# Optimization experiments

Hardware: AMD Instinct MI355X
Metric: run time of the kernel (lower is better)

Reference implementation:

```python
import jax, jax.numpy as jnp
import numpy as np

B, L, D = 2, 4096, 1024
H, DK, DV = 4, 256, 256
CONV_K, FIR_S, FIR_L = 4, 3, 31
CHUNK = 32
EPS = 1e-5


def l2norm(x):
    return x * jax.lax.rsqrt(jnp.sum(x * x, -1, keepdims=True) + 1e-6)


def causal_dwconv(x, w):
    # x: [B, L, C], w: [C, K] depthwise causal FIR conv (left pad K-1)
    C, K = w.shape
    y = jax.lax.conv_general_dilated(
        jnp.swapaxes(x, 1, 2), w[:, None, :], (1,), [(K - 1, 0)],
        feature_group_count=C, dimension_numbers=('NCH', 'OIH', 'NCH'))
    return jnp.swapaxes(y, 1, 2)


def delta_rule_chunkwise(q, k, v, beta, chunk=CHUNK):
    # q,k: [b,h,L,dk], v: [b,h,L,dv], beta: [b,h,L]
    b, h, Lx, dk = q.shape
    dv = v.shape[-1]
    pad = (-Lx) % chunk
    if pad:
        q, k, v = (jnp.pad(t, ((0, 0), (0, 0), (0, pad), (0, 0))) for t in (q, k, v))
        beta = jnp.pad(beta, ((0, 0), (0, 0), (0, pad)))
    Lp = Lx + pad
    n = Lp // chunk
    q = l2norm(q)
    k = l2norm(k)
    v = v * beta[..., None]
    k_beta = k * beta[..., None]
    ch = lambda t: t.reshape(b, h, n, chunk, -1)
    qc, kc, vc, kbc = map(ch, (q, k, v, k_beta))
    # UT transform: T = (I + strictly_lower(k_beta @ k^T))^{-1}
    A = jnp.einsum('bhncd,bhned->bhnce', kbc, kc)
    eye = jnp.eye(chunk, dtype=q.dtype)
    T = jnp.linalg.inv(eye + jnp.tril(A, -1))  # same math as the sequential forward-substitution loop
    u = T @ vc      # [b,h,n,c,dv]
    w = T @ kbc     # [b,h,n,c,dk]
    tri = jnp.tril(jnp.ones((chunk, chunk), bool))  # causal incl. diagonal

    def body(S, inp):
        q_i, k_i, u_i, w_i = inp
        attn = jnp.where(tri, jnp.einsum('bhcd,bhed->bhce', q_i, k_i), 0.)
        u_i = u_i - w_i @ S
        o_i = q_i @ S + attn @ u_i
        S = S + jnp.einsum('bhcd,bhce->bhde', k_i, u_i)
        return S, o_i

    mv = lambda t: jnp.moveaxis(t, 2, 0)
    S0 = jnp.zeros((b, h, dk, dv), q.dtype)
    S, o = jax.lax.scan(body, S0, (mv(qc), mv(kc), mv(u), mv(w)))
    o = jnp.moveaxis(o, 0, 2).reshape(b, h, Lp, dv)[:, :, :Lx]
    return o, S


def setup_inputs() -> dict:
    key = jax.random.key(0)
    ks = jax.random.split(key, 16)
    s = 0.02
    fir_short = jnp.zeros((H, DV, FIR_S)).at[..., -1].set(1.0) + 1e-3 * jax.random.normal(ks[8], (H, DV, FIR_S))
    fir_long = jnp.zeros((H, DV, FIR_L)).at[..., -1].set(1.0) + 1e-3 * jax.random.normal(ks[9], (H, DV, FIR_L))
    bl = jnp.zeros((H, 3)).at[:, 0].set(2.0).reshape(-1)  # value_path_bias
    return dict(
        hidden_states=jax.random.normal(ks[0], (B, L, D), jnp.float32),
        Wq=s * jax.random.normal(ks[1], (D, H * DK)),
        Wk=s * jax.random.normal(ks[2], (D, H * DK)),
        Wv=s * jax.random.normal(ks[3], (D, H * DV)),
        conv_q=0.3 * jax.random.normal(ks[4], (H * DK, CONV_K)),
        conv_k=0.3 * jax.random.normal(ks[5], (H * DK, CONV_K)),
        conv_v=0.3 * jax.random.normal(ks[6], (H * DV, CONV_K)),
        Wb=s * jax.random.normal(ks[7], (D, H)),
        fir_short=fir_short,
        fir_long=fir_long,
        Wg=s * jax.random.normal(ks[10], (D, H)),
        bg=0.5 * jnp.ones((H,)),  # global_gate_bias
        Wl=s * jax.random.normal(ks[11], (D, H * 3)),
        bl=bl,
        log_temp=jnp.ones((H,)),  # log(e * temp_init) with temp_init=1
        rms_w=jnp.ones((DV,)),
        Wo=s * jax.random.normal(ks[12], (H * DV, D)),
    )


def reference(hidden_states, Wq, Wk, Wv, conv_q, conv_k, conv_v, Wb,
              fir_short, fir_long, Wg, bg, Wl, bl, log_temp, rms_w, Wo):
    x = hidden_states
    Bx, Lx, _ = x.shape
    # q/k/v projections + causal short conv + SiLU (qk_activation='silu')
    q = jax.nn.silu(causal_dwconv(x @ Wq, conv_q)).reshape(Bx, Lx, H, DK)
    k = jax.nn.silu(causal_dwconv(x @ Wk, conv_k)).reshape(Bx, Lx, H, DK)
    v = jax.nn.silu(causal_dwconv(x @ Wv, conv_v)).reshape(Bx, Lx, H, DV)
    beta = jax.nn.sigmoid(x @ Wb)  # [B,L,H]
    o_d, S = delta_rule_chunkwise(
        q.transpose(0, 2, 1, 3), k.transpose(0, 2, 1, 3),
        v.transpose(0, 2, 1, 3), beta.transpose(0, 2, 1))
    delta_out = o_d.transpose(0, 2, 1, 3)  # [B,L,H,DV]
    # local FIR paths on v (per-head depthwise causal FIR)
    vf = v.reshape(Bx, Lx, H * DV)
    local_short = causal_dwconv(vf, fir_short.reshape(H * DV, FIR_S)).reshape(Bx, Lx, H, DV)
    local_long = causal_dwconv(vf, fir_long.reshape(H * DV, FIR_L)).reshape(Bx, Lx, H, DV)
    # hierarchical two-stage gating with learnable per-head temperature
    w_global = jax.nn.sigmoid(x @ Wg + bg)  # [B,L,H]
    temp = jnp.exp(log_temp)                # [H]
    logits = (x @ Wl + bl).reshape(Bx, Lx, H, 3) / temp[:, None]
    p = jax.nn.softmax(logits, axis=-1)
    local_mix = p[..., 0:1] * v + p[..., 1:2] * local_short + p[..., 2:3] * local_long
    o = w_global[..., None] * delta_out + (1.0 - w_global)[..., None] * local_mix
    # per-head RMSNorm then output projection
    o = o * jax.lax.rsqrt(jnp.mean(o * o, -1, keepdims=True) + EPS) * rms_w
    return o.reshape(Bx, Lx, H * DV) @ Wo
```

## Files before the change

### kernel.cpp

```cpp
#include <hip/hip_runtime.h>
#include <hip/hip_bf16.h>
#include <math.h>

#define Bn 2
#define Ln 4096
#define Dn 1024
#define Hn 4
#define DKn 256
#define DVn 256
#define NCHn 128

typedef __attribute__((ext_vector_type(8))) short short8;
typedef __attribute__((ext_vector_type(4))) float f32x4;

__device__ __forceinline__ float sigmoidf_(float x) { return 1.f / (1.f + __expf(-x)); }

__device__ __forceinline__ unsigned short f2bf(float f) {
  union { float f; unsigned u; } v; v.f = f;
  unsigned r = v.u + 0x7FFFu + ((v.u >> 16) & 1u);
  return (unsigned short)(r >> 16);
}

__device__ __forceinline__ float bf2f(unsigned short u) {
  union { unsigned u; float f; } v; v.u = ((unsigned)u) << 16;
  return v.f;
}

__device__ __forceinline__ unsigned cvt_pk_bf16(float a, float b) {
  unsigned r;
  asm volatile("v_cvt_pk_bf16_f32 %0, %1, %2" : "=v"(r) : "v"(a), "v"(b));
  return r;
}

__device__ __forceinline__ short8 pack_i4(int4 o) {
  short8 r;
  __builtin_memcpy(&r, &o, 16);
  return r;
}

__device__ __forceinline__ void gl2lds16(const void* g, void* l) {
  __builtin_amdgcn_global_load_lds((const __attribute__((address_space(1))) unsigned int*)g,
                                   (__attribute__((address_space(3))) unsigned int*)l, 16, 0, 0);
}

__global__ __launch_bounds__(256) void wt_all_kernel(
    const float* __restrict__ W0, const float* __restrict__ W1,
    const float* __restrict__ W2, const float* __restrict__ W3,
    unsigned short* __restrict__ T0, unsigned short* __restrict__ T1,
    unsigned short* __restrict__ T2, unsigned short* __restrict__ T3) {
  const float* W = (blockIdx.z == 0) ? W0 : (blockIdx.z == 1) ? W1
                   : (blockIdx.z == 2) ? W2 : W3;
  unsigned short* Wt = (blockIdx.z == 0) ? T0 : (blockIdx.z == 1) ? T1
                       : (blockIdx.z == 2) ? T2 : T3;
  __shared__ float tile[32][33];
  const int bx = blockIdx.x * 32;
  const int by = blockIdx.y * 32;
  const int tx = threadIdx.x & 31, ty4 = (threadIdx.x >> 5) * 4;
#pragma unroll
  for (int r = 0; r < 4; ++r)
    tile[ty4 + r][tx] = W[(size_t)(by + ty4 + r) * 1024 + bx + tx];
  __syncthreads();
#pragma unroll
  for (int r = 0; r < 4; ++r)
    Wt[(size_t)(bx + ty4 + r) * 1024 + by + tx] = f2bf(tile[tx][ty4 + r]);
}

template <int OBF>
__global__ __launch_bounds__(256, 2) void gemm_bf16(const unsigned short* __restrict__ A,
                                                    const unsigned short* __restrict__ Bt,
                                                    void* __restrict__ Cv,
                                                    int M, int N, int K) {
  __shared__ __align__(16) unsigned short As[128 * 32];
  __shared__ __align__(16) unsigned short Bs[128 * 32];
  const int tid = threadIdx.x;
  const int wid = tid >> 6, lane = tid & 63;
  const int row0 = blockIdx.y * 128, col0 = blockIdx.x * 128;
  const int wr64 = (wid >> 1) * 64, wc64 = (wid & 1) * 64;
  const int fr = lane & 15, fg = lane >> 4;
  f32x4 acc[4][4];
#pragma unroll
  for (int i = 0; i < 4; ++i)
#pragma unroll
    for (int j = 0; j < 4; ++j) acc[i][j] = (f32x4){0.f, 0.f, 0.f, 0.f};
  for (int k0 = 0; k0 < K; k0 += 32) {
#pragma unroll
    for (int i = 0; i < 2; ++i) {
      const int off = wid * 2048 + i * 1024 + (lane << 4);
      const int r = off >> 6;
      const int kb = off & 63;
      gl2lds16((const char*)A + ((size_t)(row0 + r) * K + k0) * 2 + kb, (char*)As + off);
      gl2lds16((const char*)Bt + ((size_t)(col0 + r) * K + k0) * 2 + kb, (char*)Bs + off);
    }
    __syncthreads();
    short8 a[4], b[4];
#pragma unroll
    for (int mi = 0; mi < 4; ++mi)
      a[mi] = *(const short8*)&As[(wr64 + mi * 16 + fr) * 32 + fg * 8];
#pragma unroll
    for (int ni = 0; ni < 4; ++ni)
      b[ni] = *(const short8*)&Bs[(wc64 + ni * 16 + fr) * 32 + fg * 8];
#pragma unroll
    for (int mi = 0; mi < 4; ++mi)
#pragma unroll
      for (int ni = 0; ni < 4; ++ni)
        acc[mi][ni] = __builtin_amdgcn_mfma_f32_16x16x32_bf16(a[mi], b[ni], acc[mi][ni], 0, 0, 0);
    __syncthreads();
  }
#pragma unroll
  for (int mi = 0; mi < 4; ++mi) {
    const int orow = row0 + wr64 + mi * 16 + fg * 4;
#pragma unroll
    for (int ni = 0; ni < 4; ++ni) {
      const int ocol = col0 + wc64 + ni * 16 + fr;
      if (OBF) {
        unsigned short* C = (unsigned short*)Cv;
#pragma unroll
        for (int r = 0; r < 4; ++r)
          C[(size_t)(orow + r) * N + ocol] = f2bf(acc[mi][ni][r]);
      } else {
        float* C = (float*)Cv;
#pragma unroll
        for (int r = 0; r < 4; ++r)
          C[(size_t)(orow + r) * N + ocol] = acc[mi][ni][r];
      }
    }
  }
}

__global__ __launch_bounds__(256) void gates_kernel(
    const float* __restrict__ x, const float* __restrict__ Wb,
    const float* __restrict__ Wg, const float* __restrict__ bg,
    const float* __restrict__ Wl, const float* __restrict__ bl,
    const float* __restrict__ log_temp, float* __restrict__ beta,
    float* __restrict__ wgl, float* __restrict__ pmix,
    unsigned short* __restrict__ xb) {
  const int wave = threadIdx.x >> 6, lane = threadIdx.x & 63;
  const int row = (blockIdx.x << 2) + wave;
  if (row >= Bn * Ln) return;
  const float* xr = x + (size_t)row * Dn;
  float acc[20];
#pragma unroll
  for (int c = 0; c < 20; ++c) acc[c] = 0.f;
#pragma unroll
  for (int i = 0; i < 4; ++i) {
    const float4 xv = *(const float4*)&xr[(lane << 2) + (i << 8)];
    ushort4 ob;
    ob.x = f2bf(xv.x); ob.y = f2bf(xv.y); ob.z = f2bf(xv.z); ob.w = f2bf(xv.w);
    *(ushort4*)&xb[(size_t)row * Dn + (i << 8) + (lane << 2)] = ob;
    const float xa[4] = {xv.x, xv.y, xv.z, xv.w};
#pragma unroll
    for (int j = 0; j < 4; ++j) {
      const int kk = (i << 8) + (lane << 2) + j;
      const float xx = xa[j];
#pragma unroll
      for (int h = 0; h < 4; ++h) acc[h] = fmaf(xx, Wb[kk * 4 + h], acc[h]);
#pragma unroll
      for (int h = 0; h < 4; ++h) acc[4 + h] = fmaf(xx, Wg[kk * 4 + h], acc[4 + h]);
#pragma unroll
      for (int c = 0; c < 12; ++c) acc[8 + c] = fmaf(xx, Wl[kk * 12 + c], acc[8 + c]);
    }
  }
#pragma unroll
  for (int c = 0; c < 20; ++c)
    for (int off = 32; off; off >>= 1) acc[c] += __shfl_down(acc[c], off);
  if (lane == 0) {
    const int b = row >> 12, l = row & (Ln - 1);
#pragma unroll
    for (int h = 0; h < 4; ++h)
      beta[((size_t)(b * Hn + h) << 12) + l] = sigmoidf_(acc[h]);
#pragma unroll
    for (int h = 0; h < 4; ++h) wgl[row * 4 + h] = sigmoidf_(acc[4 + h] + bg[h]);
#pragma unroll
    for (int h = 0; h < 4; ++h) {
      const float it = 1.f / __expf(log_temp[h]);
      const float l0 = (acc[8 + h * 3 + 0] + bl[h * 3 + 0]) * it;
      const float l1 = (acc[8 + h * 3 + 1] + bl[h * 3 + 1]) * it;
      const float l2 = (acc[8 + h * 3 + 2] + bl[h * 3 + 2]) * it;
      const float mx = fmaxf(l0, fmaxf(l1, l2));
      const float e0 = __expf(l0 - mx), e1 = __expf(l1 - mx), e2 = __expf(l2 - mx);
      const float is = 1.f / (e0 + e1 + e2);
      pmix[row * 12 + h * 3 + 0] = e0 * is;
      pmix[row * 12 + h * 3 + 1] = e1 * is;
      pmix[row * 12 + h * 3 + 2] = e2 * is;
    }
  }
}

#define CLT 16
__global__ __launch_bounds__(384) void conv_fused_kernel(
    const unsigned short* __restrict__ qkv, const float* __restrict__ cq,
    const float* __restrict__ ck, const float* __restrict__ cv,
    unsigned short* __restrict__ qn, unsigned short* __restrict__ kn,
    unsigned short* __restrict__ vn) {
  const int wgid = ((int)blockIdx.x & 7) * 64 + ((int)blockIdx.x >> 3);
  const int b = wgid >> 8;
  const int lt = wgid & 255;
  const int l0 = lt * CLT;
  const int t = threadIdx.x;
  const int tensor = t >> 7;
  const int head = (t & 127) >> 5;
  const int ch0 = (t & 31) * 8;
  const int col = tensor * 1024 + head * 256 + ch0;
  const float* cw = (tensor == 0) ? cq : (tensor == 1) ? ck : cv;
  float w4[8][4];
#pragma unroll
  for (int e = 0; e < 8; ++e)
#pragma unroll
    for (int j = 0; j < 4; ++j) w4[e][j] = cw[(head * 256 + ch0 + e) * 4 + j];
  float h0[8], h1[8], h2[8];
#pragma unroll
  for (int e = 0; e < 8; ++e) { h0[e] = 0.f; h1[e] = 0.f; h2[e] = 0.f; }
  {
    const int ls0 = l0 - 3;
    if (ls0 >= 0) {
      const short8 r = *(const short8*)&qkv[(((size_t)b << 12) + ls0) * 3072 + col];
#pragma unroll
      for (int e = 0; e < 8; ++e) h0[e] = bf2f((unsigned short)r[e]);
    }
    if (l0 - 2 >= 0) {
      const short8 r = *(const short8*)&qkv[(((size_t)b << 12) + l0 - 2) * 3072 + col];
#pragma unroll
      for (int e = 0; e < 8; ++e) h1[e] = bf2f((unsigned short)r[e]);
    }
    if (l0 - 1 >= 0) {
      const short8 r = *(const short8*)&qkv[(((size_t)b << 12) + l0 - 1) * 3072 + col];
#pragma unroll
      for (int e = 0; e < 8; ++e) h2[e] = bf2f((unsigned short)r[e]);
    }
  }
  unsigned short* outp = (tensor == 0) ? qn : (tensor == 1) ? kn : vn;
  const size_t obase = (((size_t)(b * Hn + head)) << 12) * 256 + ch0;
#pragma unroll
  for (int i = 0; i < CLT; ++i) {
    const int l = l0 + i;
    const short8 r = *(const short8*)&qkv[(((size_t)b << 12) + l) * 3072 + col];
    float cur[8], a[8];
#pragma unroll
    for (int e = 0; e < 8; ++e) cur[e] = bf2f((unsigned short)r[e]);
    float ssq = 0.f;
#pragma unroll
    for (int e = 0; e < 8; ++e) {
      float s = w4[e][3] * cur[e];
      s = fmaf(w4[e][0], h0[e], s);
      s = fmaf(w4[e][1], h1[e], s);
      s = fmaf(w4[e][2], h2[e], s);
      const float y = s * sigmoidf_(s);
      a[e] = y;
      ssq = fmaf(y, y, ssq);
      h0[e] = h1[e]; h1[e] = h2[e]; h2[e] = cur[e];
    }
    float sc = 1.f;
    if (tensor < 2) {
#pragma unroll
      for (int m = 1; m <= 16; m <<= 1) ssq += __shfl_xor(ssq, m);
      sc = rsqrtf(ssq + 1e-6f);
    }
    short8 o;
#pragma unroll
    for (int e = 0; e < 8; ++e) o[e] = (short)f2bf(a[e] * sc);
    *(short8*)&outp[obase + (size_t)l * 256] = o;
  }
}

__global__ __launch_bounds__(256, 2) void precomp_kernel(
    const unsigned short* __restrict__ q, const unsigned short* __restrict__ k,
    const unsigned short* __restrict__ v, const float* __restrict__ beta,
    unsigned short* __restrict__ wfrag, unsigned short* __restrict__ qfrag,
    unsigned short* __restrict__ ktfrag, unsigned short* __restrict__ afrag,
    float* __restrict__ u0frag) {
  const int blk = blockIdx.x;
  const int n = blk & 127, bh = blk >> 7;
  const size_t base = (((size_t)bh << 12) + (n << 5)) * 256;
  const size_t cid = (size_t)(bh * NCHn + n);
  __shared__ __align__(16) unsigned short ksb[32][264];
  __shared__ __align__(16) unsigned short qsb[32][264];
  __shared__ __align__(16) unsigned short vbb[32][264];
  __shared__ float Tm[32][33], Am[32][33], bet[32];
  __shared__ __align__(16) float attn_l[32][36];
  const int t = threadIdx.x;
  const int wid = t >> 6, lane = t & 63;
  const int fr = lane & 15, fg = lane >> 4;
  if (t < 32) bet[t] = beta[((size_t)bh << 12) + (n << 5) + t];
#pragma unroll
  for (int it = 0; it < 4; ++it) {
    const int idx = t + it * 256;
    const int r = idx >> 5, c8 = (idx & 31) << 3;
    const float bv = beta[((size_t)bh << 12) + (n << 5) + r];
    *(int4*)&qsb[r][c8] = *(const int4*)&q[base + r * 256 + c8];
    *(int4*)&ksb[r][c8] = *(const int4*)&k[base + r * 256 + c8];
    const int4 vv = *(const int4*)&v[base + r * 256 + c8];
    const unsigned vu[4] = {(unsigned)vv.x, (unsigned)vv.y, (unsigned)vv.z, (unsigned)vv.w};
    int4 ov;
    ov.x = cvt_pk_bf16(bf2f((unsigned short)(vu[0] & 0xffff)) * bv,
                       bf2f((unsigned short)(vu[0] >> 16)) * bv);
    ov.y = cvt_pk_bf16(bf2f((unsigned short)(vu[1] & 0xffff)) * bv,
                       bf2f((unsigned short)(vu[1] >> 16)) * bv);
    ov.z = cvt_pk_bf16(bf2f((unsigned short)(vu[2] & 0xffff)) * bv,
                       bf2f((unsigned short)(vu[2] >> 16)) * bv);
    ov.w = cvt_pk_bf16(bf2f((unsigned short)(vu[3] & 0xffff)) * bv,
                       bf2f((unsigned short)(vu[3] >> 16)) * bv);
    *(int4*)&vbb[r][c8] = ov;
  }
  __syncthreads();
  {
    const int ti = wid >> 1, tj = wid & 1;
    f32x4 G = (f32x4){0.f, 0.f, 0.f, 0.f};
    f32x4 At = (f32x4){0.f, 0.f, 0.f, 0.f};
#pragma unroll
    for (int kw = 0; kw < 8; ++kw) {
      const short8 krow = *(const short8*)&ksb[ti * 16 + fr][kw * 32 + fg * 8];
      const short8 kcol = *(const short8*)&ksb[tj * 16 + fr][kw * 32 + fg * 8];
      const short8 qrow = *(const short8*)&qsb[ti * 16 + fr][kw * 32 + fg * 8];
      G = __builtin_amdgcn_mfma_f32_16x16x32_bf16(krow, kcol, G, 0, 0, 0);
      At = __builtin_amdgcn_mfma_f32_16x16x32_bf16(qrow, kcol, At, 0, 0, 0);
    }
#pragma unroll
    for (int r_ = 0; r_ < 4; ++r_) {
      const int i = ti * 16 + fg * 4 + r_;
      const int j = tj * 16 + fr;
      Am[i][j] = bet[i] * G[r_];
      attn_l[i][j] = (j <= i) ? At[r_] : 0.f;
    }
  }
#pragma unroll
  for (int it = 0; it < 4; ++it) {
    const int u = it * 4 + wid;
    const int mi = u >> 3, kw = u & 7;
    *(int4*)&qfrag[cid * 8192 + u * 512 + lane * 8] =
        *(const int4*)&qsb[mi * 16 + fr][kw * 32 + fg * 8];
  }
#pragma unroll
  for (int it = 0; it < 4; ++it) {
    const int mi = it * 4 + wid;
    const int dk = mi * 16 + fr;
    unsigned short e[8];
#pragma unroll
    for (int j = 0; j < 8; ++j) e[j] = ksb[fg * 8 + j][dk];
    int4 o;
    o.x = e[0] | ((unsigned)e[1] << 16);
    o.y = e[2] | ((unsigned)e[3] << 16);
    o.z = e[4] | ((unsigned)e[5] << 16);
    o.w = e[6] | ((unsigned)e[7] << 16);
    *(int4*)&ktfrag[cid * 8192 + mi * 512 + lane * 8] = o;
  }
  __syncthreads();
  if (t >= 128) {
    const int mi = (t >> 6) - 2;
    const int c = mi * 16 + fr;
    const float4 a = *(const float4*)&attn_l[c][fg * 8];
    const float4 b2 = *(const float4*)&attn_l[c][fg * 8 + 4];
    int4 o;
    o.x = f2bf(a.x) | ((unsigned)f2bf(a.y) << 16);
    o.y = f2bf(a.z) | ((unsigned)f2bf(a.w) << 16);
    o.z = f2bf(b2.x) | ((unsigned)f2bf(b2.y) << 16);
    o.w = f2bf(b2.z) | ((unsigned)f2bf(b2.w) << 16);
    *(int4*)&afrag[cid * 1024 + mi * 512 + lane * 8] = o;
  }
  if (t < 32) {
    float Tcol[32];
    Tcol[0] = (t == 0) ? 1.f : 0.f;
#pragma unroll
    for (int i = 1; i < 32; ++i) {
      float s0 = 0.f, s1 = 0.f;
      int m = 0;
#pragma unroll
      for (; m + 2 <= i; m += 2) {
        s0 = fmaf(Am[i][m], Tcol[m], s0);
        s1 = fmaf(Am[i][m + 1], Tcol[m + 1], s1);
      }
      if (m < i) s0 = fmaf(Am[i][m], Tcol[m], s0);
      Tcol[i] = ((i == t) ? 1.f : 0.f) - s0 - s1;
    }
#pragma unroll
    for (int i = 0; i < 32; ++i) Tm[i][t] = Tcol[i];
  }
  __syncthreads();
  {
    float betr[8];
#pragma unroll
    for (int j = 0; j < 8; ++j) betr[j] = bet[fg * 8 + j];
    short8 Tf[2], Tbf[2];
#pragma unroll
    for (int mi = 0; mi < 2; ++mi) {
      float tv[8];
#pragma unroll
      for (int j = 0; j < 8; ++j) tv[j] = Tm[mi * 16 + fr][fg * 8 + j];
      int4 p, pb;
      p.x = cvt_pk_bf16(tv[0], tv[1]); p.y = cvt_pk_bf16(tv[2], tv[3]);
      p.z = cvt_pk_bf16(tv[4], tv[5]); p.w = cvt_pk_bf16(tv[6], tv[7]);
      pb.x = cvt_pk_bf16(tv[0] * betr[0], tv[1] * betr[1]);
      pb.y = cvt_pk_bf16(tv[2] * betr[2], tv[3] * betr[3]);
      pb.z = cvt_pk_bf16(tv[4] * betr[4], tv[5] * betr[5]);
      pb.w = cvt_pk_bf16(tv[6] * betr[6], tv[7] * betr[7]);
      Tf[mi] = pack_i4(p);
      Tbf[mi] = pack_i4(pb);
    }
    const f32x4 zero = (f32x4){0.f, 0.f, 0.f, 0.f};
#pragma unroll
    for (int tt = 0; tt < 4; ++tt) {
      const int tjc = wid * 4 + tt;
      unsigned short ev[8], ek[8];
#pragma unroll
      for (int j = 0; j < 8; ++j) {
        ev[j] = vbb[fg * 8 + j][tjc * 16 + fr];
        ek[j] = ksb[fg * 8 + j][tjc * 16 + fr];
      }
      int4 pv, pk;
      pv.x = ev[0] | ((unsigned)ev[1] << 16); pv.y = ev[2] | ((unsigned)ev[3] << 16);
      pv.z = ev[4] | ((unsigned)ev[5] << 16); pv.w = ev[6] | ((unsigned)ev[7] << 16);
      pk.x = ek[0] | ((unsigned)ek[1] << 16); pk.y = ek[2] | ((unsigned)ek[3] << 16);
      pk.z = ek[4] | ((unsigned)ek[5] << 16); pk.w = ek[6] | ((unsigned)ek[7] << 16);
      const short8 vbf = pack_i4(pv);
      const short8 kbf = pack_i4(pk);
#pragma unroll
      for (int mi = 0; mi < 2; ++mi) {
        const f32x4 U = __builtin_amdgcn_mfma_f32_16x16x32_bf16(Tf[mi], vbf, zero, 0, 0, 0);
        *(f32x4*)&u0frag[cid * 8192 + (tjc * 2 + mi) * 256 + lane * 4] = U;
        const f32x4 W = __builtin_amdgcn_mfma_f32_16x16x32_bf16(Tbf[mi], kbf, zero, 0, 0, 0);
#pragma unroll
        for (int r_ = 0; r_ < 4; ++r_)
          qsb[mi * 16 + fg * 4 + r_][tjc * 16 + fr] = f2bf(W[r_]);
      }
    }
  }
  __syncthreads();
#pragma unroll
  for (int it = 0; it < 4; ++it) {
    const int u = it * 4 + wid;
    const int mi = u >> 3, kw = u & 7;
    *(int4*)&wfrag[cid * 8192 + u * 512 + lane * 8] =
        *(const int4*)&qsb[mi * 16 + fr][kw * 32 + fg * 8];
  }
}

__global__ __launch_bounds__(128, 1) void scan_mfma(
    const unsigned short* __restrict__ wfrag, const unsigned short* __restrict__ qfrag,
    const unsigned short* __restrict__ ktfrag, const unsigned short* __restrict__ afrag,
    const float* __restrict__ u0frag, unsigned short* __restrict__ dout) {
  const int bh = blockIdx.x & 7;
  const int dvs = blockIdx.x >> 3;
  const int tid = threadIdx.x;
  const int w = tid >> 6;
  const int lane = tid & 63;
  const int fr = lane & 15, fg = lane >> 4;
  const int swz = (fr & 7) << 4;
  __shared__ __align__(16) unsigned short St[2][2048];
  __shared__ __align__(16) unsigned short ut2[2][512];
  __shared__ __align__(16) float pux[2][2][2][256];
  __shared__ __align__(16) float pox[2][2][2][256];
  f32x4 S[8];
#pragma unroll
  for (int i = 0; i < 8; ++i) S[i] = (f32x4){0.f, 0.f, 0.f, 0.f};

  const unsigned short* wbase = wfrag + (size_t)(bh * NCHn) * 8192;
  const unsigned short* qbase = qfrag + (size_t)(bh * NCHn) * 8192;
  const unsigned short* kbase = ktfrag + (size_t)(bh * NCHn) * 8192;
  const unsigned short* abase = afrag + (size_t)(bh * NCHn) * 1024;
  const float* ubase = u0frag + (size_t)(bh * NCHn) * 8192 + dvs * 512;

  short8 wr[8], qr[8], ktr[8];
  short8 ar[2] = {};
  f32x4 u0r[2];
#pragma unroll
  for (int u8 = 0; u8 < 8; ++u8) {
    const int mi = u8 >> 2, kwp = u8 & 3;
    const int u = mi * 8 + 4 * w + kwp;
    wr[u8] = *(const short8*)&wbase[u * 512 + lane * 8];
    qr[u8] = *(const short8*)&qbase[u * 512 + lane * 8];
    ktr[u8] = *(const short8*)&kbase[(8 * w + u8) * 512 + lane * 8];
  }
#pragma unroll
  for (int u = 0; u < 2; ++u) u0r[u] = *(const f32x4*)&ubase[u * 256 + lane * 4];
  if (w == 0) {
#pragma unroll
    for (int u = 0; u < 2; ++u) ar[u] = *(const short8*)&abase[u * 512 + lane * 8];
  }

  for (int n = 0; n < NCHn; ++n) {
    const int np = (n + 1 < NCHn) ? (n + 1) : n;
    const int buf = n & 1;
#pragma unroll
    for (int mi = 0; mi < 8; ++mi) {
      const unsigned w0 = cvt_pk_bf16(S[mi][0], S[mi][1]);
      const unsigned w1 = cvt_pk_bf16(S[mi][2], S[mi][3]);
      const int a = (fr * 256 + mi * 32 + fg * 8) ^ swz;
      *(uint2*)((char*)&St[w][0] + a) = make_uint2(w0, w1);
    }
    short8 sb[4];
#pragma unroll
    for (int kwp = 0; kwp < 4; ++kwp) {
      const int a = (fr * 256 + kwp * 64 + fg * 16) ^ swz;
      sb[kwp] = *(const short8*)((const char*)&St[w][0] + a);
    }
    f32x4 up[2], oq[2];
    up[0] = up[1] = (f32x4){0.f, 0.f, 0.f, 0.f};
    oq[0] = oq[1] = (f32x4){0.f, 0.f, 0.f, 0.f};
#pragma unroll
    for (int kwp = 0; kwp < 4; ++kwp) {
#pragma unroll
      for (int mi = 0; mi < 2; ++mi) {
        up[mi] = __builtin_amdgcn_mfma_f32_16x16x32_bf16(wr[mi * 4 + kwp], sb[kwp], up[mi], 0, 0, 0);
        oq[mi] = __builtin_amdgcn_mfma_f32_16x16x32_bf16(qr[mi * 4 + kwp], sb[kwp], oq[mi], 0, 0, 0);
      }
    }
    {
      const unsigned short* wp = wbase + (size_t)np * 8192;
      const unsigned short* qp = qbase + (size_t)np * 8192;
#pragma unroll
      for (int u8 = 0; u8 < 8; ++u8) {
        const int mi = u8 >> 2, kwp = u8 & 3;
        const int u = mi * 8 + 4 * w + kwp;
        wr[u8] = *(const short8*)&wp[u * 512 + lane * 8];
        qr[u8] = *(const short8*)&qp[u * 512 + lane * 8];
      }
    }
#pragma unroll
    for (int mi = 0; mi < 2; ++mi) {
      *(f32x4*)&pux[w][buf][mi][lane * 4] = up[mi];
      *(f32x4*)&pox[w][buf][mi][lane * 4] = oq[mi];
    }
    asm volatile("s_waitcnt lgkmcnt(0)" ::: "memory");
    __builtin_amdgcn_s_barrier();
    __builtin_amdgcn_sched_barrier(0);
    f32x4 o_f[2];
#pragma unroll
    for (int mi = 0; mi < 2; ++mi) {
      const f32x4 puo = *(const f32x4*)&pux[w ^ 1][buf][mi][lane * 4];
      const f32x4 uu = u0r[mi] - up[mi] - puo;
      const unsigned a0 = cvt_pk_bf16(uu[0], uu[1]);
      const unsigned a1 = cvt_pk_bf16(uu[2], uu[3]);
      const int ad = (fr * 64 + mi * 32 + fg * 8) ^ swz;
      *(uint2*)((char*)&ut2[w][0] + ad) = make_uint2(a0, a1);
      o_f[mi] = oq[mi] + *(const f32x4*)&pox[w ^ 1][buf][mi][lane * 4];
    }
    asm volatile("s_waitcnt lgkmcnt(0)" ::: "memory");
    __builtin_amdgcn_sched_barrier(0);
    const short8 ub = *(const short8*)((const char*)&ut2[w][0] + ((fr * 64 + fg * 16) ^ swz));
    if (w == 0) {
#pragma unroll
      for (int mi = 0; mi < 2; ++mi)
        o_f[mi] = __builtin_amdgcn_mfma_f32_16x16x32_bf16(ar[mi], ub, o_f[mi], 0, 0, 0);
      const unsigned short* ap = abase + (size_t)np * 1024;
#pragma unroll
      for (int u = 0; u < 2; ++u) ar[u] = *(const short8*)&ap[u * 512 + lane * 8];
      const size_t cb = ((size_t)((bh << 12) + (n << 5))) * 256;
#pragma unroll
      for (int mi = 0; mi < 2; ++mi)
#pragma unroll
        for (int r = 0; r < 4; ++r)
          dout[cb + (size_t)(mi * 16 + fg * 4 + r) * 256 + dvs * 16 + fr] = f2bf(o_f[mi][r]);
    }
    {
      const float* up_ = ubase + (size_t)np * 8192;
#pragma unroll
      for (int u = 0; u < 2; ++u) u0r[u] = *(const f32x4*)&up_[u * 256 + lane * 4];
    }
#pragma unroll
    for (int mi = 0; mi < 8; ++mi)
      S[mi] = __builtin_amdgcn_mfma_f32_16x16x32_bf16(ktr[mi], ub, S[mi], 0, 0, 0);
    {
      const unsigned short* kp = kbase + (size_t)np * 8192;
#pragma unroll
      for (int u8 = 0; u8 < 8; ++u8)
        ktr[u8] = *(const short8*)&kp[(8 * w + u8) * 512 + lane * 8];
    }
  }
}

#define MIX_LT 16
__global__ __launch_bounds__(256) void mix_kernel(
    const unsigned short* __restrict__ v, const unsigned short* __restrict__ delta,
    const float* __restrict__ wgl, const float* __restrict__ pmix,
    const float* __restrict__ firs, const float* __restrict__ firl,
    const float* __restrict__ rms_w, unsigned short* __restrict__ out) {
  const int wgid = ((int)blockIdx.x & 7) * 256 + ((int)blockIdx.x >> 3);
  const int b = wgid >> 10;
  const int h = (wgid >> 8) & 3;
  const int lt = wgid & 255;
  const int l0 = lt * MIX_LT;
  const int t = threadIdx.x;
  const int wv = t >> 6, lane = t & 63;
  const unsigned short* vcol = v + ((((size_t)(b * Hn + h)) << 12)) * 256 + t;
  const unsigned short* dcol = delta + ((((size_t)(b * Hn + h)) << 12)) * 256 + t;
  float fw[31], fs3[3];
#pragma unroll
  for (int j = 0; j < 31; ++j) fw[j] = firl[((h << 8) + t) * 31 + j];
#pragma unroll
  for (int j = 0; j < 3; ++j) fs3[j] = firs[((h << 8) + t) * 3 + j];
  const float rw = rms_w[t];
  float vbuf[46];
#pragma unroll
  for (int j = 0; j < 30; ++j) {
    const int ls = l0 - 30 + j;
    vbuf[j] = (ls >= 0) ? bf2f(vcol[(size_t)ls * 256]) : 0.f;
  }
#pragma unroll
  for (int i = 0; i < MIX_LT; ++i) vbuf[30 + i] = bf2f(vcol[(size_t)(l0 + i) * 256]);
  __shared__ float wred[MIX_LT * 4];
  float o[MIX_LT];
#pragma unroll
  for (int i = 0; i < MIX_LT; ++i) {
    const int l = l0 + i;
    const float vnew = vbuf[30 + i];
    float lo = fw[30] * vnew;
#pragma unroll
    for (int j = 0; j < 30; ++j) lo = fmaf(fw[j], vbuf[i + j], lo);
    float sh = fs3[2] * vnew;
    sh = fmaf(fs3[1], vbuf[i + 29], sh);
    sh = fmaf(fs3[0], vbuf[i + 28], sh);
    const int row = (b << 12) + l;
    const float p0 = pmix[row * 12 + h * 3 + 0];
    const float p1 = pmix[row * 12 + h * 3 + 1];
    const float p2 = pmix[row * 12 + h * 3 + 2];
    const float wg = wgl[row * 4 + h];
    const float mixv = p0 * vnew + p1 * sh + p2 * lo;
    const float oo = wg * bf2f(dcol[(size_t)l * 256]) + (1.f - wg) * mixv;
    o[i] = oo;
    float ss = oo * oo;
#pragma unroll
    for (int m = 1; m < 64; m <<= 1) ss += __shfl_xor(ss, m);
    if (lane == 0) wred[i * 4 + wv] = ss;
  }
  __syncthreads();
#pragma unroll
  for (int i = 0; i < MIX_LT; ++i) {
    const float sum = wred[i * 4] + wred[i * 4 + 1] + wred[i * 4 + 2] + wred[i * 4 + 3];
    const float sc = rsqrtf(sum * (1.f / 256.f) + 1e-5f);
    const int l = l0 + i;
    out[(size_t)((b << 12) + l) * 1024 + (h << 8) + t] = f2bf(o[i] * sc * rw);
  }
}

extern "C" void kernel_launch(void* const* d_in, const int* in_sizes, int n_in,
                              void* d_out, int out_size, void* d_ws, size_t ws_size,
                              hipStream_t stream) {
  const float* x = (const float*)d_in[0];
  const float* Wq = (const float*)d_in[1];
  const float* Wk = (const float*)d_in[2];
  const float* Wv = (const float*)d_in[3];
  const float* cq = (const float*)d_in[4];
  const float* ck = (const float*)d_in[5];
  const float* cv = (const float*)d_in[6];
  const float* Wb = (const float*)d_in[7];
  const float* firs = (const float*)d_in[8];
  const float* firl = (const float*)d_in[9];
  const float* Wg = (const float*)d_in[10];
  const float* bg = (const float*)d_in[11];
  const float* Wl = (const float*)d_in[12];
  const float* bl = (const float*)d_in[13];
  const float* ltemp = (const float*)d_in[14];
  const float* rmsw = (const float*)d_in[15];
  const float* Wo = (const float*)d_in[16];

  float* ws = (float*)d_ws;
  const size_t NE = (size_t)Bn * Ln * 1024;
  unsigned short* qkvbf = (unsigned short*)ws;
  unsigned short* wfrag = (unsigned short*)ws;
  unsigned short* qfrag = wfrag + 8388608;
  unsigned short* ktfrag = (unsigned short*)(ws + NE);
  unsigned short* afrag = ktfrag + 8388608;
  float* u0frag = ws + 2 * NE;
  unsigned short* xb = (unsigned short*)(ws + 3 * NE);
  unsigned short* normed_bf = xb;
  unsigned short* Wqt = xb + NE;
  unsigned short* Wkt = Wqt + 1048576;
  unsigned short* Wvt = Wkt + 1048576;
  unsigned short* qn_bf = (unsigned short*)(ws + 4 * NE);
  unsigned short* kn_bf = qn_bf + NE;
  unsigned short* vn_bf = (unsigned short*)(ws + 5 * NE);
  unsigned short* dout_bf = vn_bf + NE;
  float* beta = ws + 6 * NE;
  float* wgl = beta + (size_t)Bn * Hn * Ln;
  float* pmix = wgl + (size_t)Bn * Ln * Hn;
  unsigned short* Wot = (unsigned short*)(pmix + (size_t)Bn * Ln * Hn * 3);

  wt_all_kernel<<<dim3(32, 32, 4), 256, 0, stream>>>(Wq, Wk, Wv, Wo,
                                                     Wqt, Wkt, Wvt, Wot);
  gates_kernel<<<Bn * Ln / 4, 256, 0, stream>>>(x, Wb, Wg, bg, Wl, bl, ltemp,
                                                beta, wgl, pmix, xb);
  gemm_bf16<1><<<dim3(24, 64), 256, 0, stream>>>(xb, Wqt, qkvbf, Bn * Ln, 3072, 1024);
  conv_fused_kernel<<<Bn * (Ln / CLT), 384, 0, stream>>>(qkvbf, cq, ck, cv,
                                                         qn_bf, kn_bf, vn_bf);
  precomp_kernel<<<Bn * Hn * NCHn, 256, 0, stream>>>(qn_bf, kn_bf, vn_bf, beta,
                                                     wfrag, qfrag, ktfrag, afrag,
                                                     u0frag);
  scan_mfma<<<128, 128, 0, stream>>>(wfrag, qfrag, ktfrag, afrag, u0frag, dout_bf);
  mix_kernel<<<Bn * Hn * (Ln / MIX_LT), 256, 0, stream>>>(
      vn_bf, dout_bf, wgl, pmix, firs, firl, rmsw, normed_bf);
  gemm_bf16<0><<<dim3(8, 64), 256, 0, stream>>>(normed_bf, Wot, (float*)d_out,
                                                Bn * Ln, 1024, 1024);
}
```

Before: 372.3 us.

## Split scan state across four waves instead of two per workgroup

The sequential chunk scan now runs with 256 threads (4 waves) per block instead of 128, so each wave owns 64 rows of the dk dimension of the state S instead of 128. Each wave therefore does half the MFMAs and fragment loads per chunk on the serial critical path. In exchange, the cross-wave partial-sum reduction through shared memory grows from one to three partner reads. Only wave 0 now gathers the output partials, and more waves must take part in each per-chunk barrier.

```diff
diff --git a/kernel.cpp b/kernel.cpp
--- a/kernel.cpp
+++ b/kernel.cpp
@@ -211,9 +211,8 @@
 #pragma unroll
   for (int e = 0; e < 8; ++e) { h0[e] = 0.f; h1[e] = 0.f; h2[e] = 0.f; }
   {
-    const int ls0 = l0 - 3;
-    if (ls0 >= 0) {
-      const short8 r = *(const short8*)&qkv[(((size_t)b << 12) + ls0) * 3072 + col];
+    if (l0 - 3 >= 0) {
+      const short8 r = *(const short8*)&qkv[(((size_t)b << 12) + l0 - 3) * 3072 + col];
 #pragma unroll
       for (int e = 0; e < 8; ++e) h0[e] = bf2f((unsigned short)r[e]);
     }
@@ -433,7 +432,7 @@
   }
 }
 
-__global__ __launch_bounds__(128, 1) void scan_mfma(
+__global__ __launch_bounds__(256, 1) void scan_mfma(
     const unsigned short* __restrict__ wfrag, const unsigned short* __restrict__ qfrag,
     const unsigned short* __restrict__ ktfrag, const unsigned short* __restrict__ afrag,
     const float* __restrict__ u0frag, unsigned short* __restrict__ dout) {
@@ -444,13 +443,13 @@
   const int lane = tid & 63;
   const int fr = lane & 15, fg = lane >> 4;
   const int swz = (fr & 7) << 4;
-  __shared__ __align__(16) unsigned short St[2][2048];
-  __shared__ __align__(16) unsigned short ut2[2][512];
-  __shared__ __align__(16) float pux[2][2][2][256];
-  __shared__ __align__(16) float pox[2][2][2][256];
-  f32x4 S[8];
-#pragma unroll
-  for (int i = 0; i < 8; ++i) S[i] = (f32x4){0.f, 0.f, 0.f, 0.f};
+  __shared__ __align__(16) unsigned short St[4][1024];
+  __shared__ __align__(16) unsigned short ut2[4][512];
+  __shared__ __align__(16) float pux[4][2][2][256];
+  __shared__ __align__(16) float pox[4][2][2][256];
+  f32x4 S[4];
+#pragma unroll
+  for (int i = 0; i < 4; ++i) S[i] = (f32x4){0.f, 0.f, 0.f, 0.f};
 
   const unsigned short* wbase = wfrag + (size_t)(bh * NCHn) * 8192;
   const unsigned short* qbase = qfrag + (size_t)(bh * NCHn) * 8192;
@@ -458,17 +457,20 @@
   const unsigned short* abase = afrag + (size_t)(bh * NCHn) * 1024;
   const float* ubase = u0frag + (size_t)(bh * NCHn) * 8192 + dvs * 512;
 
-  short8 wr[8], qr[8], ktr[8];
+  short8 wr[2][2], qr[2][2], ktr[4];
   short8 ar[2] = {};
   f32x4 u0r[2];
 #pragma unroll
-  for (int u8 = 0; u8 < 8; ++u8) {
-    const int mi = u8 >> 2, kwp = u8 & 3;
-    const int u = mi * 8 + 4 * w + kwp;
-    wr[u8] = *(const short8*)&wbase[u * 512 + lane * 8];
-    qr[u8] = *(const short8*)&qbase[u * 512 + lane * 8];
-    ktr[u8] = *(const short8*)&kbase[(8 * w + u8) * 512 + lane * 8];
-  }
+  for (int mi2 = 0; mi2 < 2; ++mi2)
+#pragma unroll
+    for (int kwp = 0; kwp < 2; ++kwp) {
+      const int u = mi2 * 8 + 2 * w + kwp;
+      wr[mi2][kwp] = *(const short8*)&wbase[u * 512 + lane * 8];
+      qr[mi2][kwp] = *(const short8*)&qbase[u * 512 + lane * 8];
+    }
+#pragma unroll
+  for (int j = 0; j < 4; ++j)
+    ktr[j] = *(const short8*)&kbase[(4 * w + j) * 512 + lane * 8];
 #pragma unroll
   for (int u = 0; u < 2; ++u) u0r[u] = *(const f32x4*)&ubase[u * 256 + lane * 4];
   if (w == 0) {
@@ -480,75 +482,84 @@
     const int np = (n + 1 < NCHn) ? (n + 1) : n;
     const int buf = n & 1;
 #pragma unroll
-    for (int mi = 0; mi < 8; ++mi) {
-      const unsigned w0 = cvt_pk_bf16(S[mi][0], S[mi][1]);
-      const unsigned w1 = cvt_pk_bf16(S[mi][2], S[mi][3]);
-      const int a = (fr * 256 + mi * 32 + fg * 8) ^ swz;
+    for (int j = 0; j < 4; ++j) {
+      const unsigned w0 = cvt_pk_bf16(S[j][0], S[j][1]);
+      const unsigned w1 = cvt_pk_bf16(S[j][2], S[j][3]);
+      const int a = (fr * 128 + j * 32 + fg * 8) ^ swz;
       *(uint2*)((char*)&St[w][0] + a) = make_uint2(w0, w1);
     }
-    short8 sb[4];
-#pragma unroll
-    for (int kwp = 0; kwp < 4; ++kwp) {
-      const int a = (fr * 256 + kwp * 64 + fg * 16) ^ swz;
+    short8 sb[2];
+#pragma unroll
+    for (int kwp = 0; kwp < 2; ++kwp) {
+      const int a = (fr * 128 + kwp * 64 + fg * 16) ^ swz;
       sb[kwp] = *(const short8*)((const char*)&St[w][0] + a);
     }
     f32x4 up[2], oq[2];
     up[0] = up[1] = (f32x4){0.f, 0.f, 0.f, 0.f};
     oq[0] = oq[1] = (f32x4){0.f, 0.f, 0.f, 0.f};
 #pragma unroll
-    for (int kwp = 0; kwp < 4; ++kwp) {
-#pragma unroll
-      for (int mi = 0; mi < 2; ++mi) {
-        up[mi] = __builtin_amdgcn_mfma_f32_16x16x32_bf16(wr[mi * 4 + kwp], sb[kwp], up[mi], 0, 0, 0);
-        oq[mi] = __builtin_amdgcn_mfma_f32_16x16x32_bf16(qr[mi * 4 + kwp], sb[kwp], oq[mi], 0, 0, 0);
+    for (int kwp = 0; kwp < 2; ++kwp) {
+#pragma unroll
+      for (int mi2 = 0; mi2 < 2; ++mi2) {
+        up[mi2] = __builtin_amdgcn_mfma_f32_16x16x32_bf16(wr[mi2][kwp], sb[kwp], up[mi2], 0, 0, 0);
+        oq[mi2] = __builtin_amdgcn_mfma_f32_16x16x32_bf16(qr[mi2][kwp], sb[kwp], oq[mi2], 0, 0, 0);
       }
     }
     {
       const unsigned short* wp = wbase + (size_t)np * 8192;
       const unsigned short* qp = qbase + (size_t)np * 8192;
 #pragma unroll
-      for (int u8 = 0; u8 < 8; ++u8) {
-        const int mi = u8 >> 2, kwp = u8 & 3;
-        const int u = mi * 8 + 4 * w + kwp;
-        wr[u8] = *(const short8*)&wp[u * 512 + lane * 8];
-        qr[u8] = *(const short8*)&qp[u * 512 + lane * 8];
-      }
-    }
-#pragma unroll
-    for (int mi = 0; mi < 2; ++mi) {
-      *(f32x4*)&pux[w][buf][mi][lane * 4] = up[mi];
-      *(f32x4*)&pox[w][buf][mi][lane * 4] = oq[mi];
+      for (int mi2 = 0; mi2 < 2; ++mi2)
+#pragma unroll
+        for (int kwp = 0; kwp < 2; ++kwp) {
+          const int u = mi2 * 8 + 2 * w + kwp;
+          wr[mi2][kwp] = *(const short8*)&wp[u * 512 + lane * 8];
+          qr[mi2][kwp] = *(const short8*)&qp[u * 512 + lane * 8];
+        }
+    }
+#pragma unroll
+    for (int mi2 = 0; mi2 < 2; ++mi2) {
+      *(f32x4*)&pux[w][buf][mi2][lane * 4] = up[mi2];
+      *(f32x4*)&pox[w][buf][mi2][lane * 4] = oq[mi2];
     }
     asm volatile("s_waitcnt lgkmcnt(0)" ::: "memory");
     __builtin_amdgcn_s_barrier();
     __builtin_amdgcn_sched_barrier(0);
     f32x4 o_f[2];
 #pragma unroll
-    for (int mi = 0; mi < 2; ++mi) {
-      const f32x4 puo = *(const f32x4*)&pux[w ^ 1][buf][mi][lane * 4];
-      const f32x4 uu = u0r[mi] - up[mi] - puo;
+    for (int mi2 = 0; mi2 < 2; ++mi2) {
+      f32x4 s = up[mi2];
+      s += *(const f32x4*)&pux[(w + 1) & 3][buf][mi2][lane * 4];
+      s += *(const f32x4*)&pux[(w + 2) & 3][buf][mi2][lane * 4];
+      s += *(const f32x4*)&pux[(w + 3) & 3][buf][mi2][lane * 4];
+      const f32x4 uu = u0r[mi2] - s;
       const unsigned a0 = cvt_pk_bf16(uu[0], uu[1]);
       const unsigned a1 = cvt_pk_bf16(uu[2], uu[3]);
-      const int ad = (fr * 64 + mi * 32 + fg * 8) ^ swz;
+      const int ad = (fr * 64 + mi2 * 32 + fg * 8) ^ swz;
       *(uint2*)((char*)&ut2[w][0] + ad) = make_uint2(a0, a1);
-      o_f[mi] = oq[mi] + *(const f32x4*)&pox[w ^ 1][buf][mi][lane * 4];
+      if (w == 0) {
+        o_f[mi2] = oq[mi2];
+        o_f[mi2] += *(const f32x4*)&pox[1][buf][mi2][lane * 4];
+        o_f[mi2] += *(const f32x4*)&pox[2][buf][mi2][lane * 4];
+        o_f[mi2] += *(const f32x4*)&pox[3][buf][mi2][lane * 4];
+      }
     }
     asm volatile("s_waitcnt lgkmcnt(0)" ::: "memory");
     __builtin_amdgcn_sched_barrier(0);
     const short8 ub = *(const short8*)((const char*)&ut2[w][0] + ((fr * 64 + fg * 16) ^ swz));
     if (w == 0) {
 #pragma unroll
-      for (int mi = 0; mi < 2; ++mi)
-        o_f[mi] = __builtin_amdgcn_mfma_f32_16x16x32_bf16(ar[mi], ub, o_f[mi], 0, 0, 0);
+      for (int mi2 = 0; mi2 < 2; ++mi2)
+        o_f[mi2] = __builtin_amdgcn_mfma_f32_16x16x32_bf16(ar[mi2], ub, o_f[mi2], 0, 0, 0);
       const unsigned short* ap = abase + (size_t)np * 1024;
 #pragma unroll
       for (int u = 0; u < 2; ++u) ar[u] = *(const short8*)&ap[u * 512 + lane * 8];
       const size_t cb = ((size_t)((bh << 12) + (n << 5))) * 256;
 #pragma unroll
-      for (int mi = 0; mi < 2; ++mi)
+      for (int mi2 = 0; mi2 < 2; ++mi2)
 #pragma unroll
         for (int r = 0; r < 4; ++r)
-          dout[cb + (size_t)(mi * 16 + fg * 4 + r) * 256 + dvs * 16 + fr] = f2bf(o_f[mi][r]);
+          dout[cb + (size_t)(mi2 * 16 + fg * 4 + r) * 256 + dvs * 16 + fr] = f2bf(o_f[mi2][r]);
     }
     {
       const float* up_ = ubase + (size_t)np * 8192;
@@ -556,13 +567,13 @@
       for (int u = 0; u < 2; ++u) u0r[u] = *(const f32x4*)&up_[u * 256 + lane * 4];
     }
 #pragma unroll
-    for (int mi = 0; mi < 8; ++mi)
-      S[mi] = __builtin_amdgcn_mfma_f32_16x16x32_bf16(ktr[mi], ub, S[mi], 0, 0, 0);
+    for (int j = 0; j < 4; ++j)
+      S[j] = __builtin_amdgcn_mfma_f32_16x16x32_bf16(ktr[j], ub, S[j], 0, 0, 0);
     {
       const unsigned short* kp = kbase + (size_t)np * 8192;
 #pragma unroll
-      for (int u8 = 0; u8 < 8; ++u8)
-        ktr[u8] = *(const short8*)&kp[(8 * w + u8) * 512 + lane * 8];
+      for (int j = 0; j < 4; ++j)
+        ktr[j] = *(const short8*)&kp[(4 * w + j) * 512 + lane * 8];
     }
   }
 }
@@ -684,7 +695,7 @@
   precomp_kernel<<<Bn * Hn * NCHn, 256, 0, stream>>>(qn_bf, kn_bf, vn_bf, beta,
                                                      wfrag, qfrag, ktfrag, afrag,
                                                      u0frag);
-  scan_mfma<<<128, 128, 0, stream>>>(wfrag, qfrag, ktfrag, afrag, u0frag, dout_bf);
+  scan_mfma<<<128, 256, 0, stream>>>(wfrag, qfrag, ktfrag, afrag, u0frag, dout_bf);
   mix_kernel<<<Bn * Hn * (Ln / MIX_LT), 256, 0, stream>>>(
       vn_bf, dout_bf, wgl, pmix, firs, firl, rmsw, normed_bf);
   gemm_bf16<0><<<dim3(8, 64), 256, 0, stream>>>(normed_bf, Wot, (float*)d_out,
```

New measurement: 380.8 us. +2.3%, slower.
